# Kernel tuning notes

Hardware: AMD Instinct MI355X
Metric: run time of the kernel (lower is better)

## Reference

```python
import jax, jax.numpy as jnp
import numpy as np

DIM = 1024
HEADS = 16
DIM_HEAD = 64
DEPTH = 12
LN_EPS = 1e-5


def setup_inputs() -> dict:
    key = jax.random.key(0)
    k1, k2, k3 = jax.random.split(key, 3)
    B, N = 4, 2048
    inner = HEADS * DIM_HEAD
    x = jax.random.normal(k1, (B, N, DIM), dtype=jnp.float32)
    ln_w = jnp.ones((DIM,), jnp.float32)
    ln_b = jnp.zeros((DIM,), jnp.float32)
    w_qkv = jax.random.normal(k2, (DIM, 3 * inner), jnp.float32) * (DIM ** -0.5)
    w_out = jax.random.normal(k3, (inner, DIM), jnp.float32) * (inner ** -0.5)
    b_out = jnp.zeros((DIM,), jnp.float32)
    return {"x": x, "ln_w": ln_w, "ln_b": ln_b, "w_qkv": w_qkv,
            "w_out": w_out, "b_out": b_out, "layer_index": 2}


def reference(x, ln_w, ln_b, w_qkv, w_out, b_out, layer_index):
    B, N, D = x.shape
    scale = DIM_HEAD ** -0.5
    # LayerNorm
    mu = jnp.mean(x, axis=-1, keepdims=True)
    var = jnp.mean(jnp.square(x - mu), axis=-1, keepdims=True)
    xn = (x - mu) * jax.lax.rsqrt(var + LN_EPS) * ln_w + ln_b
    # QKV projection (no bias), split heads: b n (h d) -> b h n d
    qkv = xn @ w_qkv  # [B, N, 3*H*Dh]
    q, k, v = jnp.split(qkv, 3, axis=-1)
    def heads(t):
        return t.reshape(B, N, HEADS, DIM_HEAD).transpose(0, 2, 1, 3)
    q, k, v = heads(q), heads(k), heads(v)
    dots = jnp.einsum('bhnd,bhmd->bhnm', q, k) * scale  # [B,H,N,N]
    if layer_index < DEPTH // 2:
        attn = jax.nn.relu(dots)
    else:
        attn = jax.nn.softmax(dots, axis=-1)
    attn = attn / N  # divide by x.shape[1]
    out = jnp.einsum('bhnm,bhmd->bhnd', attn, v)
    out = out.transpose(0, 2, 1, 3).reshape(B, N, HEADS * DIM_HEAD)
    # to_out (heads > 1): Linear + (inactive) dropout
    return out @ w_out + b_out
```

## Files before the change

### kernel.cpp

```cpp
#include <hip/hip_runtime.h>
#include <stdint.h>

typedef __bf16 bf16x8 __attribute__((ext_vector_type(8)));
typedef __bf16 bf16x4 __attribute__((ext_vector_type(4)));
typedef short short4s __attribute__((ext_vector_type(4)));
typedef float f32x4 __attribute__((ext_vector_type(4)));

#define PSCALE (0.125f / 2048.0f)

#define GLOAD16(src, dst)                                                      \
  __builtin_amdgcn_global_load_lds(                                            \
      (__attribute__((address_space(1))) void*)const_cast<__bf16*>(src),       \
      (__attribute__((address_space(3))) void*)(dst), 16, 0, 0)

__global__ __launch_bounds__(256) void ln_fused(const float* __restrict__ x,
                                                const float* __restrict__ w,
                                                const float* __restrict__ b,
                                                __bf16* __restrict__ xn) {
  const int row = blockIdx.x;
  const int t = threadIdx.x;
  const float4 v = ((const float4*)(x + (size_t)row * 1024))[t];
  float s = v.x + v.y + v.z + v.w;
  float ss = v.x * v.x + v.y * v.y + v.z * v.z + v.w * v.w;
#pragma unroll
  for (int o = 32; o; o >>= 1) {
    s += __shfl_down(s, o);
    ss += __shfl_down(ss, o);
  }
  __shared__ float red[8];
  if ((t & 63) == 0) {
    red[t >> 6] = s;
    red[4 + (t >> 6)] = ss;
  }
  __syncthreads();
  const float tot = red[0] + red[1] + red[2] + red[3];
  const float tot2 = red[4] + red[5] + red[6] + red[7];
  const float mu = tot * (1.0f / 1024.0f);
  const float var = tot2 * (1.0f / 1024.0f) - mu * mu;
  const float rs = rsqrtf(var + 1e-5f);
  const float4 wv = ((const float4*)w)[t];
  const float4 bv = ((const float4*)b)[t];
  bf16x4 o;
  o[0] = (__bf16)((v.x - mu) * rs * wv.x + bv.x);
  o[1] = (__bf16)((v.y - mu) * rs * wv.y + bv.y);
  o[2] = (__bf16)((v.z - mu) * rs * wv.z + bv.z);
  o[3] = (__bf16)((v.w - mu) * rs * wv.w + bv.w);
  ((bf16x4*)xn)[(size_t)row * 256 + t] = o;
}

__global__ __launch_bounds__(256) void transpose_cvt(const float* __restrict__ A,
                                                     __bf16* __restrict__ At,
                                                     int R, int C) {
  __shared__ __bf16 T[64][72];
  const int rb = blockIdx.y * 64, cb = blockIdx.x * 64;
  const int tid = threadIdx.x;
  const int r = tid >> 2, cg = tid & 3;
#pragma unroll
  for (int k = 0; k < 4; ++k) {
    const float4 v =
        *(const float4*)(A + (size_t)(rb + r) * C + cb + cg * 16 + k * 4);
    T[cg * 16 + k * 4 + 0][r] = (__bf16)v.x;
    T[cg * 16 + k * 4 + 1][r] = (__bf16)v.y;
    T[cg * 16 + k * 4 + 2][r] = (__bf16)v.z;
    T[cg * 16 + k * 4 + 3][r] = (__bf16)v.w;
  }
  __syncthreads();
#pragma unroll
  for (int i = 0; i < 2; ++i) {
    const int j = i * 256 + tid;
    const int c = j >> 3, s8 = j & 7;
    const bf16x8 o = *(const bf16x8*)&T[c][s8 * 8];
    *(bf16x8*)(At + (size_t)(cb + c) * R + rb + s8 * 8) = o;
  }
}

__device__ __forceinline__ void stage_128x64(const __bf16* __restrict__ g,
                                             int ld, __bf16* lds) {
  const int lane = threadIdx.x & 63, w = threadIdx.x >> 6;
#pragma unroll
  for (int i = 0; i < 4; ++i) {
    const int j = i * 256 + w * 64 + lane;
    const int row = j >> 3, slot = j & 7;
    const __bf16* src = g + (size_t)row * ld + ((slot ^ (row & 7)) << 3);
    GLOAD16(src, lds + (size_t)(i * 256 + w * 64) * 8);
  }
}

__device__ __forceinline__ void stage_vt(const __bf16* __restrict__ g,
                                         __bf16* lds) {
  const int lane = threadIdx.x & 63, w = threadIdx.x >> 6;
#pragma unroll
  for (int i = 0; i < 4; ++i) {
    const int j = i * 256 + w * 64 + lane;
    const int d = j >> 4, slot = j & 15;
    const __bf16* src = g + (size_t)d * 2048 + ((slot ^ (d & 15)) << 3);
    GLOAD16(src, lds + (size_t)(i * 256 + w * 64) * 8);
  }
}

template <int MODE>
__global__ __launch_bounds__(256) void gemm_nt(
    const __bf16* __restrict__ A, const __bf16* __restrict__ B, int K,
    float* __restrict__ outF, __bf16* __restrict__ Qo, __bf16* __restrict__ Ko,
    __bf16* __restrict__ Vto, const float* __restrict__ bias) {
  __shared__ __bf16 As[128 * 64];
  __shared__ __bf16 Bs[128 * 64];
  const int lane = threadIdx.x & 63, w = threadIdx.x >> 6;
  const int rb = blockIdx.y * 128, cb = blockIdx.x * 128;
  const int wr = (w >> 1) * 64, wc = (w & 1) * 64;
  f32x4 acc[4][4] = {};
  const __bf16* Ab = A + (size_t)rb * K;
  const __bf16* Bb = B + (size_t)cb * K;
  const int nkb = K >> 6;
  for (int kb = 0; kb < nkb; ++kb) {
    stage_128x64(Ab + kb * 64, K, As);
    stage_128x64(Bb + kb * 64, K, Bs);
    __syncthreads();
#pragma unroll
    for (int ks = 0; ks < 2; ++ks) {
      bf16x8 af[4], bfr[4];
      const int kc = ks * 4 + (lane >> 4);
#pragma unroll
      for (int rt = 0; rt < 4; ++rt) {
        const int lr = wr + rt * 16 + (lane & 15);
        af[rt] = *(const bf16x8*)(As + lr * 64 + ((kc ^ (lr & 7)) << 3));
      }
#pragma unroll
      for (int ct = 0; ct < 4; ++ct) {
        const int lc = wc + ct * 16 + (lane & 15);
        bfr[ct] = *(const bf16x8*)(Bs + lc * 64 + ((kc ^ (lc & 7)) << 3));
      }
#pragma unroll
      for (int rt = 0; rt < 4; ++rt)
#pragma unroll
        for (int ct = 0; ct < 4; ++ct)
          acc[rt][ct] = __builtin_amdgcn_mfma_f32_16x16x32_bf16(
              af[rt], bfr[ct], acc[rt][ct], 0, 0, 0);
    }
    __syncthreads();
  }
  const int r0 = rb + wr + (lane >> 4) * 4;
  if (MODE == 1) {
#pragma unroll
    for (int ct = 0; ct < 4; ++ct) {
      const int col = cb + wc + ct * 16 + (lane & 15);
      const float bv = bias[col];
#pragma unroll
      for (int rt = 0; rt < 4; ++rt) {
        const int row = r0 + rt * 16;
#pragma unroll
        for (int r = 0; r < 4; ++r)
          outF[(size_t)(row + r) * 1024 + col] = acc[rt][ct][r] + bv;
      }
    }
  } else {
#pragma unroll
    for (int ct = 0; ct < 4; ++ct) {
      const int col = cb + wc + ct * 16 + (lane & 15);
      const int part = col >> 10, rem = col & 1023;
      const int h = rem >> 6, d = rem & 63;
#pragma unroll
      for (int rt = 0; rt < 4; ++rt) {
        const int row = r0 + rt * 16;
        const int bi = row >> 11, n = row & 2047;
        const size_t bh = (size_t)bi * 16 + h;
        if (part == 2) {
          bf16x4 pv;
#pragma unroll
          for (int r = 0; r < 4; ++r) pv[r] = (__bf16)acc[rt][ct][r];
          *(bf16x4*)(Vto + (bh * 64 + d) * 2048 + n) = pv;
        } else if (part == 0) {
          __bf16* dst = Qo + (bh * 2048 + n) * 64 + d;
#pragma unroll
          for (int r = 0; r < 4; ++r)
            dst[(size_t)r * 64] = (__bf16)(acc[rt][ct][r] * PSCALE);
        } else {
          __bf16* dst = Ko + (bh * 2048 + n) * 64 + d;
#pragma unroll
          for (int r = 0; r < 4; ++r) dst[(size_t)r * 64] = (__bf16)acc[rt][ct][r];
        }
      }
    }
  }
}

__global__ __launch_bounds__(256) void attn_relu(
    const __bf16* __restrict__ Q, const __bf16* __restrict__ K,
    const __bf16* __restrict__ Vt, __bf16* __restrict__ O) {
  __shared__ __bf16 Ks[2][128 * 64];
  __shared__ __bf16 Vs[2][64 * 128];
  const int lane = threadIdx.x & 63, w = threadIdx.x >> 6;
  const int g = lane >> 4, c15 = lane & 15;
  const int bh = blockIdx.x, qb = blockIdx.y;
  const __bf16* Qg = Q + ((size_t)bh * 2048 + qb * 256) * 64;
  const __bf16* Kg = K + (size_t)bh * 2048 * 64;
  const __bf16* Vg = Vt + (size_t)bh * 64 * 2048;

  bf16x8 qf[4][2];
#pragma unroll
  for (int rt = 0; rt < 4; ++rt)
#pragma unroll
    for (int ks = 0; ks < 2; ++ks) {
      const int row = w * 64 + rt * 16 + c15;
      qf[rt][ks] = *(const bf16x8*)(Qg + row * 64 + ks * 32 + (g << 3));
    }
  f32x4 oacc[4][4] = {};

  stage_128x64(Kg, 64, Ks[0]);
  stage_vt(Vg, Vs[0]);

  for (int kb = 0; kb < 16; ++kb) {
    const int cur = kb & 1;
    if (kb < 15) {
      stage_128x64(Kg + (size_t)(kb + 1) * 128 * 64, 64, Ks[cur ^ 1]);
      stage_vt(Vg + (kb + 1) * 128, Vs[cur ^ 1]);
      asm volatile("s_waitcnt vmcnt(8)" ::: "memory");
    } else {
      asm volatile("s_waitcnt vmcnt(0)" ::: "memory");
    }
    __builtin_amdgcn_s_barrier();
    const __bf16* __restrict__ Kc = Ks[cur];
    const __bf16* __restrict__ Vc = Vs[cur];
#pragma unroll
    for (int ct = 0; ct < 8; ++ct) {
      const int kr = ct * 16 + c15;
      const bf16x8 kf0 = *(const bf16x8*)(Kc + kr * 64 + ((g ^ (kr & 7)) << 3));
      const bf16x8 kf1 =
          *(const bf16x8*)(Kc + kr * 64 + (((4 + g) ^ (kr & 7)) << 3));
      f32x4 s[4] = {{}, {}, {}, {}};
#pragma unroll
      for (int rt = 0; rt < 4; ++rt) {
        s[rt] = __builtin_amdgcn_mfma_f32_16x16x32_bf16(kf0, qf[rt][0], s[rt],
                                                        0, 0, 0);
        s[rt] = __builtin_amdgcn_mfma_f32_16x16x32_bf16(kf1, qf[rt][1], s[rt],
                                                        0, 0, 0);
      }
      short4s pa[4];
#pragma unroll
      for (int rt = 0; rt < 4; ++rt) {
        bf16x4 p;
#pragma unroll
        for (int r = 0; r < 4; ++r) p[r] = (__bf16)fmaxf(s[rt][r], 0.0f);
        pa[rt] = __builtin_bit_cast(short4s, p);
      }
      const int vchunk = 2 * ct + (g >> 1);
#pragma unroll
      for (int dt = 0; dt < 4; ++dt) {
        const int d = dt * 16 + c15;
        const bf16x4 vfr = *(const bf16x4*)(
            Vc + d * 128 + (((vchunk ^ c15) << 3) + 4 * (g & 1)));
        const short4s vb = __builtin_bit_cast(short4s, vfr);
#pragma unroll
        for (int rt = 0; rt < 4; ++rt)
          oacc[rt][dt] = __builtin_amdgcn_mfma_f32_16x16x16bf16_1k(
              pa[rt], vb, oacc[rt][dt], 0, 0, 0);
      }
    }
    __builtin_amdgcn_s_barrier();
  }
  const int bi = bh >> 4, h = bh & 15;
#pragma unroll
  for (int rt = 0; rt < 4; ++rt)
#pragma unroll
    for (int dt = 0; dt < 4; ++dt) {
      const int col = h * 64 + dt * 16 + c15;
      const int n0 = qb * 256 + w * 64 + rt * 16 + g * 4;
      __bf16* dst = O + ((size_t)bi * 2048 + n0) * 1024 + col;
#pragma unroll
      for (int r = 0; r < 4; ++r) dst[(size_t)r * 1024] = (__bf16)oacc[rt][dt][r];
    }
}

extern "C" void kernel_launch(void* const* d_in, const int* in_sizes, int n_in,
                              void* d_out, int out_size, void* d_ws,
                              size_t ws_size, hipStream_t stream) {
  (void)in_sizes; (void)n_in; (void)out_size; (void)ws_size;
  const float* x = (const float*)d_in[0];
  const float* ln_w = (const float*)d_in[1];
  const float* ln_b = (const float*)d_in[2];
  const float* w_qkv = (const float*)d_in[3];
  const float* w_out = (const float*)d_in[4];
  const float* b_out = (const float*)d_in[5];
  char* ws = (char*)d_ws;
  __bf16* xn = (__bf16*)(ws);
  __bf16* Wt1 = (__bf16*)(ws + (size_t)(16u << 20));
  __bf16* Wt2 = (__bf16*)(ws + (size_t)(22u << 20));
  __bf16* Qb = (__bf16*)(ws + (size_t)(24u << 20));
  __bf16* Kb = (__bf16*)(ws + (size_t)(40u << 20));
  __bf16* Vtb = (__bf16*)(ws + (size_t)(56u << 20));
  __bf16* Ob = (__bf16*)(ws + (size_t)(72u << 20));
  float* out = (float*)d_out;

  ln_fused<<<8192, 256, 0, stream>>>(x, ln_w, ln_b, xn);
  transpose_cvt<<<dim3(48, 16), 256, 0, stream>>>(w_qkv, Wt1, 1024, 3072);
  transpose_cvt<<<dim3(16, 16), 256, 0, stream>>>(w_out, Wt2, 1024, 1024);
  gemm_nt<0><<<dim3(24, 64), 256, 0, stream>>>(xn, Wt1, 1024, nullptr, Qb, Kb,
                                               Vtb, nullptr);
  attn_relu<<<dim3(64, 8), 256, 0, stream>>>(Qb, Kb, Vtb, Ob);
  gemm_nt<1><<<dim3(8, 64), 256, 0, stream>>>(Ob, Wt2, 1024, out, nullptr,
                                              nullptr, nullptr, b_out);
}
```

Before: 189.8 us.

## Use 16x16x32 MFMA for PV by permuting K rows at staging

K rows are loaded into LDS in permuted order, so two adjacent 16-row score tiles together form the 32-wide K-dimension fragment that the 16x16x32 bf16 MFMA expects for P·V. The P·V product then uses half as many MFMA instructions and 16-byte V fragment loads instead of 8-byte ones. The cost is more complex address arithmetic during staging, and correctness depends on the permutation matching the MFMA operand lane layout exactly.

Measured after the change: 175.6 us. 7.5% less time.

```diff
diff --git a/kernel.cpp b/kernel.cpp
--- a/kernel.cpp
+++ b/kernel.cpp
@@ -3,7 +3,6 @@
 
 typedef __bf16 bf16x8 __attribute__((ext_vector_type(8)));
 typedef __bf16 bf16x4 __attribute__((ext_vector_type(4)));
-typedef short short4s __attribute__((ext_vector_type(4)));
 typedef float f32x4 __attribute__((ext_vector_type(4)));
 
 #define PSCALE (0.125f / 2048.0f)
@@ -86,6 +85,20 @@
   }
 }
 
+__device__ __forceinline__ void stage_k_perm(const __bf16* __restrict__ g,
+                                             __bf16* lds) {
+  const int lane = threadIdx.x & 63, w = threadIdx.x >> 6;
+#pragma unroll
+  for (int i = 0; i < 4; ++i) {
+    const int j = i * 256 + w * 64 + lane;
+    const int row = j >> 3, slot = j & 7;
+    const int srcrow =
+        (row & 96) | ((row & 12) << 1) | ((row & 16) >> 2) | (row & 3);
+    const __bf16* src = g + (size_t)srcrow * 64 + ((slot ^ (row & 7)) << 3);
+    GLOAD16(src, lds + (size_t)(i * 256 + w * 64) * 8);
+  }
+}
+
 __device__ __forceinline__ void stage_vt(const __bf16* __restrict__ g,
                                          __bf16* lds) {
   const int lane = threadIdx.x & 63, w = threadIdx.x >> 6;
@@ -206,13 +219,13 @@
     }
   f32x4 oacc[4][4] = {};
 
-  stage_128x64(Kg, 64, Ks[0]);
+  stage_k_perm(Kg, Ks[0]);
   stage_vt(Vg, Vs[0]);
 
   for (int kb = 0; kb < 16; ++kb) {
     const int cur = kb & 1;
     if (kb < 15) {
-      stage_128x64(Kg + (size_t)(kb + 1) * 128 * 64, 64, Ks[cur ^ 1]);
+      stage_k_perm(Kg + (size_t)(kb + 1) * 128 * 64, Ks[cur ^ 1]);
       stage_vt(Vg + (kb + 1) * 128, Vs[cur ^ 1]);
       asm volatile("s_waitcnt vmcnt(8)" ::: "memory");
     } else {
@@ -222,37 +235,52 @@
     const __bf16* __restrict__ Kc = Ks[cur];
     const __bf16* __restrict__ Vc = Vs[cur];
 #pragma unroll
-    for (int ct = 0; ct < 8; ++ct) {
-      const int kr = ct * 16 + c15;
-      const bf16x8 kf0 = *(const bf16x8*)(Kc + kr * 64 + ((g ^ (kr & 7)) << 3));
-      const bf16x8 kf1 =
-          *(const bf16x8*)(Kc + kr * 64 + (((4 + g) ^ (kr & 7)) << 3));
-      f32x4 s[4] = {{}, {}, {}, {}};
-#pragma unroll
-      for (int rt = 0; rt < 4; ++rt) {
-        s[rt] = __builtin_amdgcn_mfma_f32_16x16x32_bf16(kf0, qf[rt][0], s[rt],
-                                                        0, 0, 0);
-        s[rt] = __builtin_amdgcn_mfma_f32_16x16x32_bf16(kf1, qf[rt][1], s[rt],
-                                                        0, 0, 0);
-      }
-      short4s pa[4];
-#pragma unroll
-      for (int rt = 0; rt < 4; ++rt) {
-        bf16x4 p;
-#pragma unroll
-        for (int r = 0; r < 4; ++r) p[r] = (__bf16)fmaxf(s[rt][r], 0.0f);
-        pa[rt] = __builtin_bit_cast(short4s, p);
-      }
-      const int vchunk = 2 * ct + (g >> 1);
+    for (int u = 0; u < 4; ++u) {
+      f32x4 sa[4] = {{}, {}, {}, {}}, sb[4] = {{}, {}, {}, {}};
+      {
+        const int kr = u * 32 + c15;
+        const bf16x8 kf0 =
+            *(const bf16x8*)(Kc + kr * 64 + ((g ^ (kr & 7)) << 3));
+        const bf16x8 kf1 =
+            *(const bf16x8*)(Kc + kr * 64 + (((4 + g) ^ (kr & 7)) << 3));
+#pragma unroll
+        for (int rt = 0; rt < 4; ++rt) {
+          sa[rt] = __builtin_amdgcn_mfma_f32_16x16x32_bf16(kf0, qf[rt][0],
+                                                           sa[rt], 0, 0, 0);
+          sa[rt] = __builtin_amdgcn_mfma_f32_16x16x32_bf16(kf1, qf[rt][1],
+                                                           sa[rt], 0, 0, 0);
+        }
+      }
+      {
+        const int kr = u * 32 + 16 + c15;
+        const bf16x8 kf0 =
+            *(const bf16x8*)(Kc + kr * 64 + ((g ^ (kr & 7)) << 3));
+        const bf16x8 kf1 =
+            *(const bf16x8*)(Kc + kr * 64 + (((4 + g) ^ (kr & 7)) << 3));
+#pragma unroll
+        for (int rt = 0; rt < 4; ++rt) {
+          sb[rt] = __builtin_amdgcn_mfma_f32_16x16x32_bf16(kf0, qf[rt][0],
+                                                           sb[rt], 0, 0, 0);
+          sb[rt] = __builtin_amdgcn_mfma_f32_16x16x32_bf16(kf1, qf[rt][1],
+                                                           sb[rt], 0, 0, 0);
+        }
+      }
+      bf16x8 pa[4];
+#pragma unroll
+      for (int rt = 0; rt < 4; ++rt)
+#pragma unroll
+        for (int r = 0; r < 4; ++r) {
+          pa[rt][r] = (__bf16)fmaxf(sa[rt][r], 0.0f);
+          pa[rt][4 + r] = (__bf16)fmaxf(sb[rt][r], 0.0f);
+        }
 #pragma unroll
       for (int dt = 0; dt < 4; ++dt) {
         const int d = dt * 16 + c15;
-        const bf16x4 vfr = *(const bf16x4*)(
-            Vc + d * 128 + (((vchunk ^ c15) << 3) + 4 * (g & 1)));
-        const short4s vb = __builtin_bit_cast(short4s, vfr);
+        const bf16x8 vb = *(const bf16x8*)(
+            Vc + d * 128 + (((4 * u + g) ^ c15) << 3));
 #pragma unroll
         for (int rt = 0; rt < 4; ++rt)
-          oacc[rt][dt] = __builtin_amdgcn_mfma_f32_16x16x16bf16_1k(
+          oacc[rt][dt] = __builtin_amdgcn_mfma_f32_16x16x32_bf16(
               pa[rt], vb, oacc[rt][dt], 0, 0, 0);
       }
     }
```

## Restructure attention kernel: 512 threads, 16x16x32 PV MFMA, permuted K staging

Applied to the files above, without the earlier changes.

The ReLU-attention kernel now runs 8 waves per block with 32 query rows each instead of 4 waves with 64 rows, lowering per-wave accumulator registers. K rows are staged into LDS in a permuted order so two 16-key tiles form one 32-wide k-slice. This lets the P·V product use the 16x16x32 bf16 MFMA with 8-element V fragment loads in place of the 16x16x16 variant. Staging pointers are precomputed and advanced incrementally, and s_setprio brackets the MFMA sections to favour matrix issue. The tradeoffs are less data reuse per wave and a correctness dependence on the row permutation matching the P fragment layout.

New measurement: 167.3 us. 11.8% less time.

```diff
diff --git a/kernel.cpp b/kernel.cpp
--- a/kernel.cpp
+++ b/kernel.cpp
@@ -3,7 +3,6 @@
 
 typedef __bf16 bf16x8 __attribute__((ext_vector_type(8)));
 typedef __bf16 bf16x4 __attribute__((ext_vector_type(4)));
-typedef short short4s __attribute__((ext_vector_type(4)));
 typedef float f32x4 __attribute__((ext_vector_type(4)));
 
 #define PSCALE (0.125f / 2048.0f)
@@ -82,18 +81,6 @@
     const int j = i * 256 + w * 64 + lane;
     const int row = j >> 3, slot = j & 7;
     const __bf16* src = g + (size_t)row * ld + ((slot ^ (row & 7)) << 3);
-    GLOAD16(src, lds + (size_t)(i * 256 + w * 64) * 8);
-  }
-}
-
-__device__ __forceinline__ void stage_vt(const __bf16* __restrict__ g,
-                                         __bf16* lds) {
-  const int lane = threadIdx.x & 63, w = threadIdx.x >> 6;
-#pragma unroll
-  for (int i = 0; i < 4; ++i) {
-    const int j = i * 256 + w * 64 + lane;
-    const int d = j >> 4, slot = j & 15;
-    const __bf16* src = g + (size_t)d * 2048 + ((slot ^ (d & 15)) << 3);
     GLOAD16(src, lds + (size_t)(i * 256 + w * 64) * 8);
   }
 }
@@ -184,37 +171,63 @@
   }
 }
 
-__global__ __launch_bounds__(256) void attn_relu(
+__global__ __launch_bounds__(512) void attn_relu(
     const __bf16* __restrict__ Q, const __bf16* __restrict__ K,
     const __bf16* __restrict__ Vt, __bf16* __restrict__ O) {
   __shared__ __bf16 Ks[2][128 * 64];
   __shared__ __bf16 Vs[2][64 * 128];
-  const int lane = threadIdx.x & 63, w = threadIdx.x >> 6;
+  const int tid = threadIdx.x;
+  const int lane = tid & 63, w = tid >> 6;
   const int g = lane >> 4, c15 = lane & 15;
   const int bh = blockIdx.x, qb = blockIdx.y;
   const __bf16* Qg = Q + ((size_t)bh * 2048 + qb * 256) * 64;
   const __bf16* Kg = K + (size_t)bh * 2048 * 64;
   const __bf16* Vg = Vt + (size_t)bh * 64 * 2048;
 
-  bf16x8 qf[4][2];
-#pragma unroll
-  for (int rt = 0; rt < 4; ++rt)
+  const __bf16* kp0;
+  const __bf16* kp1;
+  const __bf16* vp0;
+  const __bf16* vp1;
+  {
+    const int j0 = tid, j1 = 512 + tid;
+    const int r0_ = j0 >> 3, s0_ = j0 & 7;
+    const int r1_ = j1 >> 3, s1_ = j1 & 7;
+    const int sr0 = (r0_ & 96) | ((r0_ & 12) << 1) | ((r0_ & 16) >> 2) | (r0_ & 3);
+    const int sr1 = (r1_ & 96) | ((r1_ & 12) << 1) | ((r1_ & 16) >> 2) | (r1_ & 3);
+    kp0 = Kg + (size_t)sr0 * 64 + ((s0_ ^ (r0_ & 7)) << 3);
+    kp1 = Kg + (size_t)sr1 * 64 + ((s1_ ^ (r1_ & 7)) << 3);
+    const int d0_ = j0 >> 4, t0_ = j0 & 15;
+    const int d1_ = j1 >> 4, t1_ = j1 & 15;
+    vp0 = Vg + (size_t)d0_ * 2048 + ((t0_ ^ (d0_ & 15)) << 3);
+    vp1 = Vg + (size_t)d1_ * 2048 + ((t1_ ^ (d1_ & 15)) << 3);
+  }
+  const int dstoff = w * 64 * 8;
+
+  bf16x8 qf[2][2];
+#pragma unroll
+  for (int rt = 0; rt < 2; ++rt)
 #pragma unroll
     for (int ks = 0; ks < 2; ++ks) {
-      const int row = w * 64 + rt * 16 + c15;
+      const int row = w * 32 + rt * 16 + c15;
       qf[rt][ks] = *(const bf16x8*)(Qg + row * 64 + ks * 32 + (g << 3));
     }
-  f32x4 oacc[4][4] = {};
-
-  stage_128x64(Kg, 64, Ks[0]);
-  stage_vt(Vg, Vs[0]);
+  f32x4 oacc[2][4] = {};
+
+  GLOAD16(kp0, Ks[0] + dstoff);
+  GLOAD16(kp1, Ks[0] + 512 * 8 + dstoff);
+  GLOAD16(vp0, Vs[0] + dstoff);
+  GLOAD16(vp1, Vs[0] + 512 * 8 + dstoff);
+  kp0 += 128 * 64; kp1 += 128 * 64; vp0 += 128; vp1 += 128;
 
   for (int kb = 0; kb < 16; ++kb) {
     const int cur = kb & 1;
     if (kb < 15) {
-      stage_128x64(Kg + (size_t)(kb + 1) * 128 * 64, 64, Ks[cur ^ 1]);
-      stage_vt(Vg + (kb + 1) * 128, Vs[cur ^ 1]);
-      asm volatile("s_waitcnt vmcnt(8)" ::: "memory");
+      GLOAD16(kp0, Ks[cur ^ 1] + dstoff);
+      GLOAD16(kp1, Ks[cur ^ 1] + 512 * 8 + dstoff);
+      GLOAD16(vp0, Vs[cur ^ 1] + dstoff);
+      GLOAD16(vp1, Vs[cur ^ 1] + 512 * 8 + dstoff);
+      kp0 += 128 * 64; kp1 += 128 * 64; vp0 += 128; vp1 += 128;
+      asm volatile("s_waitcnt vmcnt(4)" ::: "memory");
     } else {
       asm volatile("s_waitcnt vmcnt(0)" ::: "memory");
     }
@@ -222,49 +235,52 @@
     const __bf16* __restrict__ Kc = Ks[cur];
     const __bf16* __restrict__ Vc = Vs[cur];
 #pragma unroll
-    for (int ct = 0; ct < 8; ++ct) {
-      const int kr = ct * 16 + c15;
-      const bf16x8 kf0 = *(const bf16x8*)(Kc + kr * 64 + ((g ^ (kr & 7)) << 3));
-      const bf16x8 kf1 =
-          *(const bf16x8*)(Kc + kr * 64 + (((4 + g) ^ (kr & 7)) << 3));
-      f32x4 s[4] = {{}, {}, {}, {}};
-#pragma unroll
-      for (int rt = 0; rt < 4; ++rt) {
-        s[rt] = __builtin_amdgcn_mfma_f32_16x16x32_bf16(kf0, qf[rt][0], s[rt],
-                                                        0, 0, 0);
-        s[rt] = __builtin_amdgcn_mfma_f32_16x16x32_bf16(kf1, qf[rt][1], s[rt],
-                                                        0, 0, 0);
-      }
-      short4s pa[4];
-#pragma unroll
-      for (int rt = 0; rt < 4; ++rt) {
-        bf16x4 p;
-#pragma unroll
-        for (int r = 0; r < 4; ++r) p[r] = (__bf16)fmaxf(s[rt][r], 0.0f);
-        pa[rt] = __builtin_bit_cast(short4s, p);
-      }
-      const int vchunk = 2 * ct + (g >> 1);
+    for (int u = 0; u < 4; ++u) {
+      const int kra = u * 32 + c15;
+      const int krb = u * 32 + 16 + c15;
+      const bf16x8 kfa0 = *(const bf16x8*)(Kc + kra * 64 + ((g ^ (kra & 7)) << 3));
+      const bf16x8 kfa1 = *(const bf16x8*)(Kc + kra * 64 + (((4 + g) ^ (kra & 7)) << 3));
+      const bf16x8 kfb0 = *(const bf16x8*)(Kc + krb * 64 + ((g ^ (krb & 7)) << 3));
+      const bf16x8 kfb1 = *(const bf16x8*)(Kc + krb * 64 + (((4 + g) ^ (krb & 7)) << 3));
+      f32x4 sa[2] = {{}, {}}, sb[2] = {{}, {}};
+      __builtin_amdgcn_s_setprio(1);
+#pragma unroll
+      for (int rt = 0; rt < 2; ++rt) {
+        sa[rt] = __builtin_amdgcn_mfma_f32_16x16x32_bf16(kfa0, qf[rt][0], sa[rt], 0, 0, 0);
+        sa[rt] = __builtin_amdgcn_mfma_f32_16x16x32_bf16(kfa1, qf[rt][1], sa[rt], 0, 0, 0);
+        sb[rt] = __builtin_amdgcn_mfma_f32_16x16x32_bf16(kfb0, qf[rt][0], sb[rt], 0, 0, 0);
+        sb[rt] = __builtin_amdgcn_mfma_f32_16x16x32_bf16(kfb1, qf[rt][1], sb[rt], 0, 0, 0);
+      }
+      __builtin_amdgcn_s_setprio(0);
+      bf16x8 pa[2];
+#pragma unroll
+      for (int rt = 0; rt < 2; ++rt)
+#pragma unroll
+        for (int r = 0; r < 4; ++r) {
+          pa[rt][r] = (__bf16)fmaxf(sa[rt][r], 0.0f);
+          pa[rt][4 + r] = (__bf16)fmaxf(sb[rt][r], 0.0f);
+        }
+      __builtin_amdgcn_s_setprio(1);
 #pragma unroll
       for (int dt = 0; dt < 4; ++dt) {
         const int d = dt * 16 + c15;
-        const bf16x4 vfr = *(const bf16x4*)(
-            Vc + d * 128 + (((vchunk ^ c15) << 3) + 4 * (g & 1)));
-        const short4s vb = __builtin_bit_cast(short4s, vfr);
-#pragma unroll
-        for (int rt = 0; rt < 4; ++rt)
-          oacc[rt][dt] = __builtin_amdgcn_mfma_f32_16x16x16bf16_1k(
+        const bf16x8 vb = *(const bf16x8*)(Vc + d * 128 + (((4 * u + g) ^ c15) << 3));
+#pragma unroll
+        for (int rt = 0; rt < 2; ++rt)
+          oacc[rt][dt] = __builtin_amdgcn_mfma_f32_16x16x32_bf16(
               pa[rt], vb, oacc[rt][dt], 0, 0, 0);
       }
+      __builtin_amdgcn_s_setprio(0);
     }
     __builtin_amdgcn_s_barrier();
   }
   const int bi = bh >> 4, h = bh & 15;
 #pragma unroll
-  for (int rt = 0; rt < 4; ++rt)
+  for (int rt = 0; rt < 2; ++rt)
 #pragma unroll
     for (int dt = 0; dt < 4; ++dt) {
       const int col = h * 64 + dt * 16 + c15;
-      const int n0 = qb * 256 + w * 64 + rt * 16 + g * 4;
+      const int n0 = qb * 256 + w * 32 + rt * 16 + g * 4;
       __bf16* dst = O + ((size_t)bi * 2048 + n0) * 1024 + col;
 #pragma unroll
       for (int r = 0; r < 4; ++r) dst[(size_t)r * 1024] = (__bf16)oacc[rt][dt][r];
@@ -296,7 +312,7 @@
   transpose_cvt<<<dim3(16, 16), 256, 0, stream>>>(w_out, Wt2, 1024, 1024);
   gemm_nt<0><<<dim3(24, 64), 256, 0, stream>>>(xn, Wt1, 1024, nullptr, Qb, Kb,
                                                Vtb, nullptr);
-  attn_relu<<<dim3(64, 8), 256, 0, stream>>>(Qb, Kb, Vtb, Ob);
+  attn_relu<<<dim3(64, 8), 512, 0, stream>>>(Qb, Kb, Vtb, Ob);
   gemm_nt<1><<<dim3(8, 64), 256, 0, stream>>>(Ob, Wt2, 1024, out, nullptr,
                                               nullptr, nullptr, b_out);
 }
```
